# Performance work log

Hardware: AMD Instinct MI355X
Metric: run time of the kernel (lower is better)

## Reference

```python
import math
import jax, jax.numpy as jnp
import numpy as np

N = 8192
IN_DIM = 512
INTER = 512
HID = 1024
OUT = 512
GROUPS = 16
EPS = 1e-5


def setup_inputs() -> dict:
    key = jax.random.key(0)
    ks = jax.random.split(key, 12)
    w = lambda k, shape: jax.random.normal(k, shape, jnp.float32) * 0.02
    return {
        "h": jax.random.normal(ks[0], (N, IN_DIM), jnp.float32),
        "D": jax.random.uniform(ks[1], (N, N), dtype=jnp.float32),
        "h_prime": jax.random.normal(ks[2], (N, OUT), jnp.float32),
        "Wq": w(ks[3], (INTER, IN_DIM)), "bq": jnp.zeros((INTER,), jnp.float32),
        "Wk": w(ks[4], (INTER, IN_DIM)), "bk": jnp.zeros((INTER,), jnp.float32),
        "Wv": w(ks[5], (INTER, IN_DIM)), "bv": jnp.zeros((INTER,), jnp.float32),
        "Wr": w(ks[6], (HID, INTER)), "br": jnp.zeros((HID,), jnp.float32),
        "Wc": w(ks[7], (HID, OUT)), "bc": jnp.zeros((HID,), jnp.float32),
        "Wp": w(ks[8], (OUT, 2 * HID)), "bp": jnp.zeros((OUT,), jnp.float32),
        "alpha": jnp.full((OUT,), 0.25, jnp.float32),       # PReLU per-channel slope
        "gamma": jnp.ones((OUT,), jnp.float32),             # GroupNorm weight
        "beta": jnp.zeros((OUT,), jnp.float32),             # GroupNorm bias
    }


def reference(h, D, h_prime, Wq, bq, Wk, bk, Wv, bv, Wr, br, Wc, bc, Wp, bp, alpha, gamma, beta):
    Q = h @ Wq.T + bq                                    # [N, inter]
    K = h @ Wk.T + bk
    V = h @ Wv.T + bv
    scores = (Q @ K.T) / math.sqrt(INTER)                # [N, N]
    attn = jax.nn.softmax(D * scores, axis=-1)           # decay-masked softmax
    h_ret = attn @ V                                     # [N, inter]
    h_ret = jax.nn.gelu(h_ret @ Wr.T + br, approximate=False)  # torch GELU (erf)
    h_cat = h_prime @ Wc.T + bc                          # [N, hid]
    x = jnp.concatenate([h_ret, h_cat], axis=-1) @ Wp.T + bp   # [N, out]
    x = jnp.where(x >= 0, x, alpha * x)                  # PReLU, per-channel
    # GroupNorm over [1, out, N]: stats per group over (channels_in_group, N)
    xT = x.T                                             # [out, N]
    grp = xT.reshape(GROUPS, (OUT // GROUPS) * N)
    mean = grp.mean(axis=1, keepdims=True)
    var = grp.var(axis=1, keepdims=True)
    grp = (grp - mean) * jax.lax.rsqrt(var + EPS)
    xT = grp.reshape(OUT, N) * gamma[:, None] + beta[:, None]
    return xT.T                                          # [N, out]
```

## Files before the change

kernel.cpp:

```cpp
#include <hip/hip_runtime.h>
#include <stdint.h>
#include <math.h>

typedef float f32x4 __attribute__((ext_vector_type(4)));
typedef __bf16 bf16x8 __attribute__((ext_vector_type(8)));
typedef unsigned int u32x4 __attribute__((ext_vector_type(4)));
typedef unsigned short u16;

#define DEVINL static __device__ __forceinline__

DEVINL u16 f2bf(float f) {
  union { float f; unsigned u; } x; x.f = f;
  unsigned r = x.u + 0x7fffu + ((x.u >> 16) & 1u);
  return (u16)(r >> 16);
}

DEVINL void gload_lds16(const void* g, void* l) {
  __builtin_amdgcn_global_load_lds(
      (__attribute__((address_space(1))) void*)(g),
      (__attribute__((address_space(3))) void*)(l), 16, 0, 0);
}

__global__ void cast_kernel(const float* __restrict__ src, u16* __restrict__ dst, int n) {
  int i = (blockIdx.x * 256 + threadIdx.x) * 4;
  if (i >= n) return;
  float4 v = *(const float4*)(src + i);
  u16 o[4] = { f2bf(v.x), f2bf(v.y), f2bf(v.z), f2bf(v.w) };
  *(uint64_t*)(dst + i) = *(uint64_t*)o;
}

template<int EPI>
__global__ __launch_bounds__(256, 2) void gemm_nt(
    const u16* __restrict__ A, int lda, const u16* __restrict__ B, int ldb,
    void* __restrict__ C, int ldc, int coff,
    const float* __restrict__ bias, const float* __restrict__ alpha,
    int N128, int K, float scale, int map)
{
  __shared__ __align__(16) u16 at[2][128 * 64];
  __shared__ __align__(16) u16 bt[2][128 * 64];
  const int tid = threadIdx.x;
  const int w = tid >> 6, lane = tid & 63, r = lane & 15, kg = lane >> 4;
  int bm, bn;
  if (map == 1) { const int x = blockIdx.x & 7, i = blockIdx.x >> 3; bm = x * 8 + (i >> 2); bn = i & 3; }
  else          { bm = blockIdx.x / N128; bn = blockIdx.x % N128; }
  const int m0 = bm * 128, n0 = bn * 128;

  f32x4 acc[4][4];
  #pragma unroll
  for (int m = 0; m < 4; ++m)
    #pragma unroll
    for (int n = 0; n < 4; ++n) acc[m][n] = f32x4{0.f, 0.f, 0.f, 0.f};

  const int srow = tid >> 3, sc = tid & 7;
  const int nk = K >> 6;

  #pragma unroll
  for (int i = 0; i < 4; ++i) {
    int row = srow + i * 32, cs = (sc ^ row) & 7;
    gload_lds16(A + (size_t)(m0 + row) * lda + cs * 8, at[0] + i * 2048 + w * 512);
    gload_lds16(B + (size_t)(n0 + row) * ldb + cs * 8, bt[0] + i * 2048 + w * 512);
  }
  __syncthreads();

  for (int kt = 0; kt < nk; ++kt) {
    const int cur = kt & 1;
    if (kt + 1 < nk) {
      #pragma unroll
      for (int i = 0; i < 4; ++i) {
        int row = srow + i * 32, cs = (sc ^ row) & 7;
        int kcol = (kt + 1) * 64 + cs * 8;
        gload_lds16(A + (size_t)(m0 + row) * lda + kcol, at[cur ^ 1] + i * 2048 + w * 512);
        gload_lds16(B + (size_t)(n0 + row) * ldb + kcol, bt[cur ^ 1] + i * 2048 + w * 512);
      }
    }
    #pragma unroll
    for (int ks = 0; ks < 2; ++ks) {
      bf16x8 af[4], bff[4];
      #pragma unroll
      for (int m = 0; m < 4; ++m) {
        int row = (w >> 1) * 64 + m * 16 + r;
        int cs = ((ks * 4 + kg) ^ row) & 7;
        af[m] = *(const bf16x8*)(at[cur] + row * 64 + cs * 8);
      }
      #pragma unroll
      for (int n = 0; n < 4; ++n) {
        int row = (w & 1) * 64 + n * 16 + r;
        int cs = ((ks * 4 + kg) ^ row) & 7;
        bff[n] = *(const bf16x8*)(bt[cur] + row * 64 + cs * 8);
      }
      #pragma unroll
      for (int m = 0; m < 4; ++m)
        #pragma unroll
        for (int n = 0; n < 4; ++n)
          acc[m][n] = __builtin_amdgcn_mfma_f32_16x16x32_bf16(af[m], bff[n], acc[m][n], 0, 0, 0);
    }
    __syncthreads();
  }

  #pragma unroll
  for (int m = 0; m < 4; ++m) {
    #pragma unroll
    for (int n = 0; n < 4; ++n) {
      const int gcol = n0 + (w & 1) * 64 + n * 16 + r;
      #pragma unroll
      for (int reg = 0; reg < 4; ++reg) {
        const int grow = m0 + (w >> 1) * 64 + m * 16 + kg * 4 + reg;
        float v = acc[m][n][reg];
        if (EPI == 0) v = (v + bias[gcol]) * scale;
        if (EPI == 1) v = v + bias[grow];
        if (EPI == 2) { v += bias[gcol]; v = 0.5f * v * (1.f + erff(v * 0.70710678118654752f)); }
        if (EPI == 5) v = v / bias[grow];
        if (EPI == 3) {
          v += bias[gcol];
          float a = alpha[gcol];
          v = (v >= 0.f) ? v : a * v;
          ((float*)C)[(size_t)grow * ldc + coff + gcol] = v;
        } else {
          ((u16*)C)[(size_t)grow * ldc + coff + gcol] = f2bf(v);
        }
      }
    }
  }
}

__global__ __launch_bounds__(256, 2) void sgemm_exp(
    const u16* __restrict__ A, const u16* __restrict__ B,
    u16* __restrict__ P, const float* __restrict__ Dmat, float* __restrict__ psum)
{
  __shared__ __align__(16) u16 at[2][128 * 64];
  __shared__ __align__(16) u16 bt[2][128 * 64];
  const int tid = threadIdx.x;
  const int w = tid >> 6, lane = tid & 63, r = lane & 15, kg = lane >> 4;
  const int xcd = blockIdx.x & 7, i = blockIdx.x >> 3;
  const int bm = (xcd >> 1) * 16 + (i & 15);
  const int bn = (xcd & 1) * 32 + (i >> 4);
  const int m0 = bm * 128, n0 = bn * 128;

  f32x4 acc[4][4];
  #pragma unroll
  for (int m = 0; m < 4; ++m)
    #pragma unroll
    for (int n = 0; n < 4; ++n) acc[m][n] = f32x4{0.f, 0.f, 0.f, 0.f};
  float dreg[64];

  const int srow = tid >> 3, sc = tid & 7;
  const int gcolb = n0 + (w & 1) * 64 + r;
  const int growb = m0 + (w >> 1) * 64 + kg * 4;

  #pragma unroll
  for (int ii = 0; ii < 4; ++ii) {
    int row = srow + ii * 32, cs = (sc ^ row) & 7;
    gload_lds16(A + (size_t)(m0 + row) * 512 + cs * 8, at[0] + ii * 2048 + w * 512);
    gload_lds16(B + (size_t)(n0 + row) * 512 + cs * 8, bt[0] + ii * 2048 + w * 512);
  }
  __syncthreads();

  #pragma unroll
  for (int kt = 0; kt < 8; ++kt) {
    const int cur = kt & 1;
    if (kt < 7) {
      #pragma unroll
      for (int ii = 0; ii < 4; ++ii) {
        int row = srow + ii * 32, cs = (sc ^ row) & 7;
        int kcol = (kt + 1) * 64 + cs * 8;
        gload_lds16(A + (size_t)(m0 + row) * 512 + kcol, at[cur ^ 1] + ii * 2048 + w * 512);
        gload_lds16(B + (size_t)(n0 + row) * 512 + kcol, bt[cur ^ 1] + ii * 2048 + w * 512);
      }
    }
    #pragma unroll
    for (int q = 0; q < 8; ++q) {
      const int id = kt * 8 + q;
      const int m = id >> 4, n = (id >> 2) & 3, reg = id & 3;
      dreg[id] = __builtin_nontemporal_load(
          Dmat + (size_t)(growb + m * 16 + reg) * 8192 + (gcolb + n * 16));
    }
    #pragma unroll
    for (int ks = 0; ks < 2; ++ks) {
      bf16x8 af[4], bff[4];
      #pragma unroll
      for (int m = 0; m < 4; ++m) {
        int row = (w >> 1) * 64 + m * 16 + r;
        int cs = ((ks * 4 + kg) ^ row) & 7;
        af[m] = *(const bf16x8*)(at[cur] + row * 64 + cs * 8);
      }
      #pragma unroll
      for (int n = 0; n < 4; ++n) {
        int row = (w & 1) * 64 + n * 16 + r;
        int cs = ((ks * 4 + kg) ^ row) & 7;
        bff[n] = *(const bf16x8*)(bt[cur] + row * 64 + cs * 8);
      }
      #pragma unroll
      for (int m = 0; m < 4; ++m)
        #pragma unroll
        for (int n = 0; n < 4; ++n)
          acc[m][n] = __builtin_amdgcn_mfma_f32_16x16x32_bf16(af[m], bff[n], acc[m][n], 0, 0, 0);
    }
    __syncthreads();
  }

  #pragma unroll
  for (int m = 0; m < 4; ++m) {
    float rs[4] = {0.f, 0.f, 0.f, 0.f};
    #pragma unroll
    for (int n = 0; n < 4; ++n) {
      const int gcol = gcolb + n * 16;
      #pragma unroll
      for (int reg = 0; reg < 4; ++reg) {
        const int grow = growb + m * 16 + reg;
        const float p = __expf(acc[m][n][reg] * dreg[m * 16 + n * 4 + reg]);
        rs[reg] += p;
        P[(size_t)grow * 8192 + gcol] = f2bf(p);
      }
    }
    #pragma unroll
    for (int reg = 0; reg < 4; ++reg) {
      float v = rs[reg];
      v += __shfl_xor(v, 1); v += __shfl_xor(v, 2);
      v += __shfl_xor(v, 4); v += __shfl_xor(v, 8);
      if (r == 0)
        psum[(size_t)(growb + m * 16 + reg) * 128 + bn * 2 + (w & 1)] = v;
    }
  }
}

__global__ __launch_bounds__(256) void rowsum_kernel(const float* __restrict__ psum,
                                                     float* __restrict__ ls) {
  const int row = blockIdx.x * 4 + (threadIdx.x >> 6);
  const int lane = threadIdx.x & 63;
  const float2 v = *(const float2*)(psum + (size_t)row * 128 + lane * 2);
  float s = v.x + v.y;
  #pragma unroll
  for (int m = 1; m < 64; m <<= 1) s += __shfl_xor(s, m);
  if (lane == 0) ls[row] = s;
}

__global__ void gn_stats_kernel(const float* __restrict__ x, float* __restrict__ part) {
  const int g = blockIdx.x >> 4, ch = blockIdx.x & 15;
  const int t = threadIdx.x;
  float s = 0.f, ss = 0.f;
  const int cl = (t & 7) * 4;
  const int r0 = ch * 512 + (t >> 3);
  for (int i = 0; i < 16; ++i) {
    const float4 v = *(const float4*)(x + (size_t)(r0 + i * 32) * 512 + g * 32 + cl);
    s += v.x + v.y + v.z + v.w;
    ss += v.x * v.x + v.y * v.y + v.z * v.z + v.w * v.w;
  }
  #pragma unroll
  for (int m = 1; m < 64; m <<= 1) { s += __shfl_xor(s, m); ss += __shfl_xor(ss, m); }
  __shared__ float red[8];
  const int w = t >> 6, lane = t & 63;
  if (lane == 0) { red[w * 2] = s; red[w * 2 + 1] = ss; }
  __syncthreads();
  if (t == 0) {
    part[blockIdx.x * 2]     = red[0] + red[2] + red[4] + red[6];
    part[blockIdx.x * 2 + 1] = red[1] + red[3] + red[5] + red[7];
  }
}

__global__ void gn_finalize_kernel(const float* __restrict__ part, float* __restrict__ mv) {
  const int g = threadIdx.x;
  if (g < 16) {
    float s = 0.f, ss = 0.f;
    for (int ch = 0; ch < 16; ++ch) {
      s  += part[(g * 16 + ch) * 2];
      ss += part[(g * 16 + ch) * 2 + 1];
    }
    const float mean = s * (1.f / 262144.f);
    const float var = ss * (1.f / 262144.f) - mean * mean;
    mv[g * 2] = mean;
    mv[g * 2 + 1] = rsqrtf(var + 1e-5f);
  }
}

__global__ void gn_norm_kernel(const float* __restrict__ x, const float* __restrict__ mv,
                               const float* __restrict__ gamma, const float* __restrict__ beta,
                               float* __restrict__ out) {
  const int idx = (blockIdx.x * 256 + threadIdx.x) * 4;
  const int c = idx & 511, g = c >> 5;
  const float mean = mv[g * 2], rs = mv[g * 2 + 1];
  float4 v = *(const float4*)(x + idx);
  const float4 gm = *(const float4*)(gamma + c);
  const float4 bt = *(const float4*)(beta + c);
  v.x = (v.x - mean) * rs * gm.x + bt.x;
  v.y = (v.y - mean) * rs * gm.y + bt.y;
  v.z = (v.z - mean) * rs * gm.z + bt.z;
  v.w = (v.w - mean) * rs * gm.w + bt.w;
  *(float4*)(out + idx) = v;
}

extern "C" void kernel_launch(void* const* d_in, const int* in_sizes, int n_in,
                              void* d_out, int out_size, void* d_ws, size_t ws_size,
                              hipStream_t stream) {
  (void)in_sizes; (void)n_in; (void)out_size; (void)ws_size;
  const float* h     = (const float*)d_in[0];
  const float* Dm    = (const float*)d_in[1];
  const float* hp    = (const float*)d_in[2];
  const float* Wq    = (const float*)d_in[3];
  const float* bq    = (const float*)d_in[4];
  const float* Wk    = (const float*)d_in[5];
  const float* bk    = (const float*)d_in[6];
  const float* Wv    = (const float*)d_in[7];
  const float* bv    = (const float*)d_in[8];
  const float* Wr    = (const float*)d_in[9];
  const float* br    = (const float*)d_in[10];
  const float* Wc    = (const float*)d_in[11];
  const float* bc    = (const float*)d_in[12];
  const float* Wp    = (const float*)d_in[13];
  const float* bp    = (const float*)d_in[14];
  const float* alpha = (const float*)d_in[15];
  const float* gamma = (const float*)d_in[16];
  const float* beta  = (const float*)d_in[17];

  char* ws = (char*)d_ws;
  const size_t MB = 1ull << 20;
  u16*   P    = (u16*)(ws);
  u16*   hb   = (u16*)(ws);
  u16*   xcat = (u16*)(ws);
  float* xf   = (float*)(ws + 32 * MB);
  u16*   hpb  = (u16*)(ws + 128 * MB);
  u16*   Qb   = (u16*)(ws + 144 * MB);
  u16*   hrb  = (u16*)(ws + 144 * MB);
  u16*   Kb   = (u16*)(ws + 152 * MB);
  u16*   VTb  = (u16*)(ws + 160 * MB);
  u16*   Wqb  = (u16*)(ws + 168 * MB);
  u16*   Wkb  = Wqb + 262144;
  u16*   Wvb  = Wkb + 262144;
  u16*   Wrb  = Wvb + 262144;
  u16*   Wcb  = Wrb + 524288;
  u16*   Wpb  = Wcb + 524288;
  float* lsum = (float*)(ws + 168 * MB + 5767168);
  float* gp   = lsum + 8192;
  float* mv   = gp + 512;
  float* psum = (float*)(ws + 176 * MB);

  cast_kernel<<<4096, 256, 0, stream>>>(h, hb, 4194304);
  cast_kernel<<<4096, 256, 0, stream>>>(hp, hpb, 4194304);
  cast_kernel<<<256, 256, 0, stream>>>(Wq, Wqb, 262144);
  cast_kernel<<<256, 256, 0, stream>>>(Wk, Wkb, 262144);
  cast_kernel<<<256, 256, 0, stream>>>(Wv, Wvb, 262144);
  cast_kernel<<<512, 256, 0, stream>>>(Wr, Wrb, 524288);
  cast_kernel<<<512, 256, 0, stream>>>(Wc, Wcb, 524288);
  cast_kernel<<<1024, 256, 0, stream>>>(Wp, Wpb, 1048576);

  gemm_nt<0><<<256, 256, 0, stream>>>(hb, 512, Wqb, 512, Qb, 512, 0, bq, nullptr, 4, 512, 0.044194173824159216f, 0);
  gemm_nt<0><<<256, 256, 0, stream>>>(hb, 512, Wkb, 512, Kb, 512, 0, bk, nullptr, 4, 512, 1.0f, 0);
  gemm_nt<1><<<256, 256, 0, stream>>>(Wvb, 512, hb, 512, VTb, 8192, 0, bv, nullptr, 64, 512, 1.0f, 0);

  sgemm_exp<<<4096, 256, 0, stream>>>(Qb, Kb, P, Dm, psum);
  rowsum_kernel<<<2048, 256, 0, stream>>>(psum, lsum);

  gemm_nt<5><<<256, 256, 0, stream>>>(P, 8192, VTb, 8192, hrb, 512, 0, lsum, nullptr, 4, 8192, 1.0f, 1);

  gemm_nt<2><<<512, 256, 0, stream>>>(hrb, 512, Wrb, 512, xcat, 2048, 0, br, nullptr, 8, 512, 1.0f, 0);
  gemm_nt<0><<<512, 256, 0, stream>>>(hpb, 512, Wcb, 512, xcat, 2048, 1024, bc, nullptr, 8, 512, 1.0f, 0);

  gemm_nt<3><<<256, 256, 0, stream>>>(xcat, 2048, Wpb, 2048, xf, 512, 0, bp, alpha, 4, 2048, 1.0f, 0);

  gn_stats_kernel<<<256, 256, 0, stream>>>(xf, gp);
  gn_finalize_kernel<<<1, 64, 0, stream>>>(gp, mv);
  gn_norm_kernel<<<4096, 256, 0, stream>>>(xf, mv, gamma, beta, (float*)d_out);
}
```

Baseline: 455.7 us.

## Split-K the P·V GEMM into four partials with separate normalizing combine kernel

Replaces the single attn·V GEMM (256 blocks over K=8192) with a split-K kernel launching 1024 blocks, each covering a quarter of K and writing fp32 partial outputs with nontemporal stores. A combine kernel sums the four partials, divides by the softmax row sum and casts to bf16. This is meant to fill the GPU with more workgroups, at the cost of extra global traffic for the fp32 partial buffers and one additional launch.

New measurement: 423.6 us. -7.0%, faster.

```diff
diff --git a/kernel.cpp b/kernel.cpp
--- a/kernel.cpp
+++ b/kernel.cpp
@@ -34,15 +34,13 @@
     const u16* __restrict__ A, int lda, const u16* __restrict__ B, int ldb,
     void* __restrict__ C, int ldc, int coff,
     const float* __restrict__ bias, const float* __restrict__ alpha,
-    int N128, int K, float scale, int map)
+    int N128, int K, float scale)
 {
   __shared__ __align__(16) u16 at[2][128 * 64];
   __shared__ __align__(16) u16 bt[2][128 * 64];
   const int tid = threadIdx.x;
   const int w = tid >> 6, lane = tid & 63, r = lane & 15, kg = lane >> 4;
-  int bm, bn;
-  if (map == 1) { const int x = blockIdx.x & 7, i = blockIdx.x >> 3; bm = x * 8 + (i >> 2); bn = i & 3; }
-  else          { bm = blockIdx.x / N128; bn = blockIdx.x % N128; }
+  const int bm = blockIdx.x / N128, bn = blockIdx.x % N128;
   const int m0 = bm * 128, n0 = bn * 128;
 
   f32x4 acc[4][4];
@@ -109,7 +107,6 @@
         if (EPI == 0) v = (v + bias[gcol]) * scale;
         if (EPI == 1) v = v + bias[grow];
         if (EPI == 2) { v += bias[gcol]; v = 0.5f * v * (1.f + erff(v * 0.70710678118654752f)); }
-        if (EPI == 5) v = v / bias[grow];
         if (EPI == 3) {
           v += bias[gcol];
           float a = alpha[gcol];
@@ -221,6 +218,102 @@
         psum[(size_t)(growb + m * 16 + reg) * 128 + bn * 2 + (w & 1)] = v;
     }
   }
+}
+
+__global__ __launch_bounds__(256, 2) void pv_split(
+    const u16* __restrict__ P, const u16* __restrict__ VT, float* __restrict__ Opart)
+{
+  __shared__ __align__(16) u16 at[2][128 * 64];
+  __shared__ __align__(16) u16 bt[2][128 * 64];
+  const int tid = threadIdx.x;
+  const int w = tid >> 6, lane = tid & 63, r = lane & 15, kg = lane >> 4;
+  const int xcd = blockIdx.x & 7, i = blockIdx.x >> 3;
+  const int bn = i & 3, ks = (i >> 2) & 3, bm = xcd * 8 + (i >> 4);
+  const int m0 = bm * 128, n0 = bn * 128;
+  const int koff = ks * 2048;
+
+  f32x4 acc[4][4];
+  #pragma unroll
+  for (int m = 0; m < 4; ++m)
+    #pragma unroll
+    for (int n = 0; n < 4; ++n) acc[m][n] = f32x4{0.f, 0.f, 0.f, 0.f};
+
+  const int srow = tid >> 3, sc = tid & 7;
+
+  #pragma unroll
+  for (int ii = 0; ii < 4; ++ii) {
+    int row = srow + ii * 32, cs = (sc ^ row) & 7;
+    gload_lds16(P  + (size_t)(m0 + row) * 8192 + koff + cs * 8, at[0] + ii * 2048 + w * 512);
+    gload_lds16(VT + (size_t)(n0 + row) * 8192 + koff + cs * 8, bt[0] + ii * 2048 + w * 512);
+  }
+  __syncthreads();
+
+  for (int kt = 0; kt < 32; ++kt) {
+    const int cur = kt & 1;
+    if (kt < 31) {
+      #pragma unroll
+      for (int ii = 0; ii < 4; ++ii) {
+        int row = srow + ii * 32, cs = (sc ^ row) & 7;
+        int kcol = koff + (kt + 1) * 64 + cs * 8;
+        gload_lds16(P  + (size_t)(m0 + row) * 8192 + kcol, at[cur ^ 1] + ii * 2048 + w * 512);
+        gload_lds16(VT + (size_t)(n0 + row) * 8192 + kcol, bt[cur ^ 1] + ii * 2048 + w * 512);
+      }
+    }
+    #pragma unroll
+    for (int ks2 = 0; ks2 < 2; ++ks2) {
+      bf16x8 af[4], bff[4];
+      #pragma unroll
+      for (int m = 0; m < 4; ++m) {
+        int row = (w >> 1) * 64 + m * 16 + r;
+        int cs = ((ks2 * 4 + kg) ^ row) & 7;
+        af[m] = *(const bf16x8*)(at[cur] + row * 64 + cs * 8);
+      }
+      #pragma unroll
+      for (int n = 0; n < 4; ++n) {
+        int row = (w & 1) * 64 + n * 16 + r;
+        int cs = ((ks2 * 4 + kg) ^ row) & 7;
+        bff[n] = *(const bf16x8*)(bt[cur] + row * 64 + cs * 8);
+      }
+      #pragma unroll
+      for (int m = 0; m < 4; ++m)
+        #pragma unroll
+        for (int n = 0; n < 4; ++n)
+          acc[m][n] = __builtin_amdgcn_mfma_f32_16x16x32_bf16(af[m], bff[n], acc[m][n], 0, 0, 0);
+    }
+    __syncthreads();
+  }
+
+  float* op = Opart + (size_t)ks * 4194304;
+  #pragma unroll
+  for (int m = 0; m < 4; ++m) {
+    #pragma unroll
+    for (int n = 0; n < 4; ++n) {
+      const int gcol = n0 + (w & 1) * 64 + n * 16 + r;
+      #pragma unroll
+      for (int reg = 0; reg < 4; ++reg) {
+        const int grow = m0 + (w >> 1) * 64 + m * 16 + kg * 4 + reg;
+        __builtin_nontemporal_store(acc[m][n][reg], op + (size_t)grow * 512 + gcol);
+      }
+    }
+  }
+}
+
+__global__ __launch_bounds__(256) void pv_combine(
+    const float* __restrict__ Opart, const float* __restrict__ ls, u16* __restrict__ hrb)
+{
+  const int idx = (blockIdx.x * 256 + threadIdx.x) * 4;
+  const int row = idx >> 9;
+  const float li = 1.f / ls[row];
+  float4 a = *(const float4*)(Opart + idx);
+  const float4 b = *(const float4*)(Opart + 4194304 + idx);
+  const float4 c = *(const float4*)(Opart + 8388608 + idx);
+  const float4 d = *(const float4*)(Opart + 12582912 + idx);
+  a.x = (a.x + b.x + c.x + d.x) * li;
+  a.y = (a.y + b.y + c.y + d.y) * li;
+  a.z = (a.z + b.z + c.z + d.z) * li;
+  a.w = (a.w + b.w + c.w + d.w) * li;
+  u16 o[4] = { f2bf(a.x), f2bf(a.y), f2bf(a.z), f2bf(a.w) };
+  *(uint64_t*)(hrb + idx) = *(uint64_t*)o;
 }
 
 __global__ __launch_bounds__(256) void rowsum_kernel(const float* __restrict__ psum,
@@ -332,6 +425,7 @@
   float* gp   = lsum + 8192;
   float* mv   = gp + 512;
   float* psum = (float*)(ws + 176 * MB);
+  float* Opart = (float*)(ws + 184 * MB);
 
   cast_kernel<<<4096, 256, 0, stream>>>(h, hb, 4194304);
   cast_kernel<<<4096, 256, 0, stream>>>(hp, hpb, 4194304);
@@ -342,19 +436,20 @@
   cast_kernel<<<512, 256, 0, stream>>>(Wc, Wcb, 524288);
   cast_kernel<<<1024, 256, 0, stream>>>(Wp, Wpb, 1048576);
 
-  gemm_nt<0><<<256, 256, 0, stream>>>(hb, 512, Wqb, 512, Qb, 512, 0, bq, nullptr, 4, 512, 0.044194173824159216f, 0);
-  gemm_nt<0><<<256, 256, 0, stream>>>(hb, 512, Wkb, 512, Kb, 512, 0, bk, nullptr, 4, 512, 1.0f, 0);
-  gemm_nt<1><<<256, 256, 0, stream>>>(Wvb, 512, hb, 512, VTb, 8192, 0, bv, nullptr, 64, 512, 1.0f, 0);
+  gemm_nt<0><<<256, 256, 0, stream>>>(hb, 512, Wqb, 512, Qb, 512, 0, bq, nullptr, 4, 512, 0.044194173824159216f);
+  gemm_nt<0><<<256, 256, 0, stream>>>(hb, 512, Wkb, 512, Kb, 512, 0, bk, nullptr, 4, 512, 1.0f);
+  gemm_nt<1><<<256, 256, 0, stream>>>(Wvb, 512, hb, 512, VTb, 8192, 0, bv, nullptr, 64, 512, 1.0f);
 
   sgemm_exp<<<4096, 256, 0, stream>>>(Qb, Kb, P, Dm, psum);
   rowsum_kernel<<<2048, 256, 0, stream>>>(psum, lsum);
 
-  gemm_nt<5><<<256, 256, 0, stream>>>(P, 8192, VTb, 8192, hrb, 512, 0, lsum, nullptr, 4, 8192, 1.0f, 1);
-
-  gemm_nt<2><<<512, 256, 0, stream>>>(hrb, 512, Wrb, 512, xcat, 2048, 0, br, nullptr, 8, 512, 1.0f, 0);
-  gemm_nt<0><<<512, 256, 0, stream>>>(hpb, 512, Wcb, 512, xcat, 2048, 1024, bc, nullptr, 8, 512, 1.0f, 0);
-
-  gemm_nt<3><<<256, 256, 0, stream>>>(xcat, 2048, Wpb, 2048, xf, 512, 0, bp, alpha, 4, 2048, 1.0f, 0);
+  pv_split<<<1024, 256, 0, stream>>>(P, VTb, Opart);
+  pv_combine<<<4096, 256, 0, stream>>>(Opart, lsum, hrb);
+
+  gemm_nt<2><<<512, 256, 0, stream>>>(hrb, 512, Wrb, 512, xcat, 2048, 0, br, nullptr, 8, 512, 1.0f);
+  gemm_nt<0><<<512, 256, 0, stream>>>(hpb, 512, Wcb, 512, xcat, 2048, 1024, bc, nullptr, 8, 512, 1.0f);
+
+  gemm_nt<3><<<256, 256, 0, stream>>>(xcat, 2048, Wpb, 2048, xf, 512, 0, bp, alpha, 4, 2048, 1.0f);
 
   gn_stats_kernel<<<256, 256, 0, stream>>>(xf, gp);
   gn_finalize_kernel<<<1, 64, 0, stream>>>(gp, mv);
```
